# Kernel optimization log

Hardware: AMD Instinct MI355X
Metric: run time of the kernel (lower is better)

Reference implementation:

```python
import jax, jax.numpy as jnp
import numpy as np

N_NODES = 100000
N_EDGES = 1600000
NFEAT, NHID, NCLASS = 128, 64, 16


def setup_inputs() -> dict:
    key = jax.random.key(0)
    k1, k2, k3, k4, k5 = jax.random.split(key, 5)
    x = jax.random.normal(k1, (N_NODES, NFEAT), dtype=jnp.float32)
    edge_index = jax.random.randint(k2, (2, N_EDGES), 0, N_NODES, dtype=jnp.int64)
    edge_weight = jax.random.uniform(k3, (N_EDGES,), dtype=jnp.float32)
    # PyG Linear default init ~ kaiming-uniform; plain scaled normals suffice as a baseline
    W1 = jax.random.normal(k4, (NFEAT, NHID), dtype=jnp.float32) / np.sqrt(NFEAT)
    W2 = jax.random.normal(k5, (NHID, NCLASS), dtype=jnp.float32) / np.sqrt(NHID)
    return {"x": x, "edge_index": edge_index, "edge_weight": edge_weight, "W1": W1, "W2": W2}


def _gcn_conv(x, W, src, dst, w, num_nodes):
    # GCNConv(normalize=False, add_self_loops=False, bias=False):
    # out[dst] = sum_{e: dst(e)=dst} w_e * (x @ W)[src(e)]
    h = x @ W                                    # [N, out]
    msg = w[:, None] * h[src]                    # [E, out] gathered messages
    return jax.ops.segment_sum(msg, dst, num_segments=num_nodes)


def reference(x, edge_index, edge_weight, W1, W2):
    src, dst = edge_index[0], edge_index[1]
    h = jax.nn.relu(_gcn_conv(x, W1, src, dst, edge_weight, N_NODES))
    out = _gcn_conv(h, W2, src, dst, edge_weight, N_NODES)
    return out
```

## Files before the change

### kernel.cpp

```cpp
#include <hip/hip_runtime.h>

#define N_NODES 100000
#define N_EDGES 1600000
#define NFEAT 128
#define NHID 64
#define NCLASS 16

#define NPB 196
#define NB 511
#define HIST_EPT 16
#define HIST_BLOCKS ((N_EDGES + 256 * HIST_EPT - 1) / (256 * HIST_EPT))
#define FILL_EPT 8
#define FILL_BLOCKS ((N_EDGES + 256 * FILL_EPT - 1) / (256 * FILL_EPT))
#define NTILES ((N_NODES + 15) / 16)
#define GEMM_BLOCKS ((NTILES + 3) / 4)

typedef unsigned int u32;
typedef __attribute__((ext_vector_type(8))) short bf16x8;
typedef __attribute__((ext_vector_type(4))) float f32x4;

__device__ __forceinline__ u32 pack_bf16(float a, float b) {
    u32 ua = __float_as_uint(a);
    u32 ub = __float_as_uint(b);
    ua = (ua + 0x7fffu + ((ua >> 16) & 1u)) >> 16;
    ub = (ub + 0x7fffu + ((ub >> 16) & 1u)) >> 16;
    return ua | (ub << 16);
}
__device__ __forceinline__ short f2bf(float f) {
    u32 u = __float_as_uint(f);
    u = (u + 0x7fffu + ((u >> 16) & 1u)) >> 16;
    return (short)u;
}
__device__ __forceinline__ float bf16_lo(u32 u) { return __uint_as_float(u << 16); }
__device__ __forceinline__ float bf16_hi(u32 u) { return __uint_as_float(u & 0xffff0000u); }

__global__ void detect_kernel(const u32* __restrict__ ei, int* __restrict__ flag) {
    __shared__ int any_nz;
    if (threadIdx.x == 0) any_nz = 0;
    __syncthreads();
    u32 v = ei[2 * threadIdx.x + 1];
    if (v != 0) any_nz = 1;
    __syncthreads();
    if (threadIdx.x == 0) *flag = any_nz;
}

__device__ __forceinline__ int load_idx(const void* ei, int flag, size_t pos) {
    return flag ? ((const int*)ei)[pos] : (int)((const long long*)ei)[pos];
}

__global__ __launch_bounds__(256) void histA_kernel(const void* __restrict__ ei,
                                                    const int* __restrict__ flag,
                                                    int* __restrict__ ghist) {
    __shared__ int cnt[512];
    int t = threadIdx.x;
    cnt[t] = 0;
    cnt[t + 256] = 0;
    __syncthreads();
    int f = *flag;
    int base = blockIdx.x * 256 * HIST_EPT;
#pragma unroll
    for (int k = 0; k < HIST_EPT; ++k) {
        int e = base + k * 256 + t;
        if (e < N_EDGES) {
            int d = load_idx(ei, f, (size_t)N_EDGES + e);
            atomicAdd(&cnt[d / NPB], 1);
        }
    }
    __syncthreads();
    if (cnt[t] > 0) atomicAdd(&ghist[t], cnt[t]);
    if (cnt[t + 256] > 0) atomicAdd(&ghist[t + 256], cnt[t + 256]);
}

__global__ __launch_bounds__(512) void scanA_kernel(const int* __restrict__ ghist,
                                                    int* __restrict__ bstart,
                                                    int* __restrict__ gcursor) {
    __shared__ int lds[512];
    int t = threadIdx.x;
    int own = (t < NB) ? ghist[t] : 0;
    lds[t] = own;
    __syncthreads();
    for (int off = 1; off < 512; off <<= 1) {
        int v = (t >= off) ? lds[t - off] : 0;
        __syncthreads();
        lds[t] += v;
        __syncthreads();
    }
    int excl = lds[t] - own;
    bstart[t] = excl;
    if (t == 511) bstart[512] = lds[511];
    if (t < NB) gcursor[t] = excl;
}

__global__ __launch_bounds__(256) void fillA_kernel(const void* __restrict__ ei,
                                                    const int* __restrict__ flag,
                                                    const float* __restrict__ ew,
                                                    int* __restrict__ gcursor,
                                                    int2* __restrict__ ebuf) {
    __shared__ int cnt[512];
    __shared__ int base[512];
    int t = threadIdx.x;
    cnt[t] = 0;
    cnt[t + 256] = 0;
    __syncthreads();
    int f = *flag;
    int eb = blockIdx.x * 256 * FILL_EPT;
    int src[FILL_EPT], bin[FILL_EPT], rank[FILL_EPT];
    float w[FILL_EPT];
#pragma unroll
    for (int k = 0; k < FILL_EPT; ++k) {
        int e = eb + k * 256 + t;
        bin[k] = -1;
        if (e < N_EDGES) {
            int s = load_idx(ei, f, (size_t)e);
            int d = load_idx(ei, f, (size_t)N_EDGES + e);
            int b = d / NPB;
            src[k] = s | ((d - b * NPB) << 20);
            w[k] = ew[e];
            bin[k] = b;
            rank[k] = atomicAdd(&cnt[b], 1);
        }
    }
    __syncthreads();
    if (cnt[t] > 0) base[t] = atomicAdd(&gcursor[t], cnt[t]);
    if (cnt[t + 256] > 0) base[t + 256] = atomicAdd(&gcursor[t + 256], cnt[t + 256]);
    __syncthreads();
#pragma unroll
    for (int k = 0; k < FILL_EPT; ++k) {
        if (bin[k] >= 0) {
            int pos = base[bin[k]] + rank[k];
            ebuf[pos] = make_int2(src[k], __float_as_int(w[k]));
        }
    }
}

__global__ __launch_bounds__(256) void sortB_kernel(const int2* __restrict__ ebuf,
                                                    const int* __restrict__ bstart,
                                                    int2* __restrict__ ebuf2,
                                                    int* __restrict__ row_ptr) {
    __shared__ int cnt[NPB];
    __shared__ int sc[256];
    __shared__ int cur[NPB];
    int t = threadIdx.x, b = blockIdx.x;
    for (int i = t; i < NPB; i += 256) cnt[i] = 0;
    __syncthreads();
    int start = bstart[b], end = bstart[b + 1];
    for (int i = start + t; i < end; i += 256) {
        int dl = ((u32)ebuf[i].x) >> 20;
        atomicAdd(&cnt[dl], 1);
    }
    __syncthreads();
    int own = (t < NPB) ? cnt[t] : 0;
    sc[t] = own;
    __syncthreads();
    for (int off = 1; off < 256; off <<= 1) {
        int v = (t >= off) ? sc[t - off] : 0;
        __syncthreads();
        sc[t] += v;
        __syncthreads();
    }
    int excl = sc[t] - own;
    if (t < NPB) {
        cur[t] = excl;
        int node = b * NPB + t;
        if (node < N_NODES) row_ptr[node] = start + excl;
    }
    if (b == 0 && t == 0) row_ptr[N_NODES] = N_EDGES;
    __syncthreads();
    for (int i = start + t; i < end; i += 256) {
        int2 p = ebuf[i];
        int dl = ((u32)p.x) >> 20;
        int pos = start + atomicAdd(&cur[dl], 1);
        ebuf2[pos] = make_int2(p.x & 0xFFFFF, p.y);
    }
}

__global__ __launch_bounds__(256) void gemm1_kernel(const float* __restrict__ X,
                                                    const float* __restrict__ W,
                                                    u32* __restrict__ Y) {
    __shared__ float Wsh[NFEAT * NHID];
    int t = threadIdx.x;
    for (int i = t; i < NFEAT * NHID; i += 256) Wsh[i] = W[i];
    __syncthreads();
    int wid = t >> 6;
    int lane = t & 63;
    int r = lane & 15, g = lane >> 4;
    int m0 = (blockIdx.x * 4 + wid) * 16;
    if (m0 >= N_NODES) return;

    bf16x8 af[4][4];
#pragma unroll
    for (int nt = 0; nt < 4; ++nt)
#pragma unroll
        for (int kt = 0; kt < 4; ++kt)
#pragma unroll
            for (int j = 0; j < 8; ++j)
                af[nt][kt][j] = f2bf(Wsh[(kt * 32 + g * 8 + j) * NHID + nt * 16 + r]);

    const float* xr = X + (size_t)(m0 + r) * NFEAT + g * 8;
    bf16x8 bfr[4];
#pragma unroll
    for (int kt = 0; kt < 4; ++kt) {
        float4 v0 = *(const float4*)(xr + kt * 32);
        float4 v1 = *(const float4*)(xr + kt * 32 + 4);
        bfr[kt][0] = f2bf(v0.x); bfr[kt][1] = f2bf(v0.y);
        bfr[kt][2] = f2bf(v0.z); bfr[kt][3] = f2bf(v0.w);
        bfr[kt][4] = f2bf(v1.x); bfr[kt][5] = f2bf(v1.y);
        bfr[kt][6] = f2bf(v1.z); bfr[kt][7] = f2bf(v1.w);
    }

    u32* yr = Y + (size_t)(m0 + r) * (NHID / 2);
#pragma unroll
    for (int nt = 0; nt < 4; ++nt) {
        f32x4 acc = {0.f, 0.f, 0.f, 0.f};
#pragma unroll
        for (int kt = 0; kt < 4; ++kt)
            acc = __builtin_amdgcn_mfma_f32_16x16x32_bf16(af[nt][kt], bfr[kt], acc, 0, 0, 0);
        uint2 o;
        o.x = pack_bf16(acc[0], acc[1]);
        o.y = pack_bf16(acc[2], acc[3]);
        *(uint2*)(yr + nt * 8 + g * 2) = o;
    }
}

__global__ __launch_bounds__(256) void gemm2_kernel(const float* __restrict__ H,
                                                    const float* __restrict__ W,
                                                    u32* __restrict__ Y) {
    __shared__ float Wsh[NHID * NCLASS];
    int t = threadIdx.x;
    for (int i = t; i < NHID * NCLASS; i += 256) Wsh[i] = W[i];
    __syncthreads();
    int wid = t >> 6;
    int lane = t & 63;
    int r = lane & 15, g = lane >> 4;
    int m0 = (blockIdx.x * 4 + wid) * 16;
    if (m0 >= N_NODES) return;

    bf16x8 af[2];
#pragma unroll
    for (int kt = 0; kt < 2; ++kt)
#pragma unroll
        for (int j = 0; j < 8; ++j)
            af[kt][j] = f2bf(Wsh[(kt * 32 + g * 8 + j) * NCLASS + r]);

    const float* hr = H + (size_t)(m0 + r) * NHID + g * 8;
    bf16x8 bfr[2];
#pragma unroll
    for (int kt = 0; kt < 2; ++kt) {
        float4 v0 = *(const float4*)(hr + kt * 32);
        float4 v1 = *(const float4*)(hr + kt * 32 + 4);
        bfr[kt][0] = f2bf(v0.x); bfr[kt][1] = f2bf(v0.y);
        bfr[kt][2] = f2bf(v0.z); bfr[kt][3] = f2bf(v0.w);
        bfr[kt][4] = f2bf(v1.x); bfr[kt][5] = f2bf(v1.y);
        bfr[kt][6] = f2bf(v1.z); bfr[kt][7] = f2bf(v1.w);
    }

    f32x4 acc = {0.f, 0.f, 0.f, 0.f};
    acc = __builtin_amdgcn_mfma_f32_16x16x32_bf16(af[0], bfr[0], acc, 0, 0, 0);
    acc = __builtin_amdgcn_mfma_f32_16x16x32_bf16(af[1], bfr[1], acc, 0, 0, 0);

    u32* yr = Y + (size_t)(m0 + r) * (NCLASS / 2);
    uint2 o;
    o.x = pack_bf16(acc[0], acc[1]);
    o.y = pack_bf16(acc[2], acc[3]);
    *(uint2*)(yr + g * 2) = o;
}

__global__ __launch_bounds__(256) void agg1_kernel(const u32* __restrict__ xwb,
                                                   const int* __restrict__ row_ptr,
                                                   const int2* __restrict__ ep,
                                                   float* __restrict__ h) {
    int t = blockIdx.x * 256 + threadIdx.x;
    int node = t >> 5;
    int ln = t & 31;
    if (node >= N_NODES) return;
    int start = row_ptr[node], end = row_ptr[node + 1];
    float a0x = 0.f, a0y = 0.f, a1x = 0.f, a1y = 0.f;
    float a2x = 0.f, a2y = 0.f, a3x = 0.f, a3y = 0.f;
    int last = end - 1;
    for (int i = start; i < end; i += 4) {
        int i1 = min(i + 1, last), i2 = min(i + 2, last), i3 = min(i + 3, last);
        int2 p0 = ep[i];
        int2 p1 = ep[i1];
        int2 p2 = ep[i2];
        int2 p3 = ep[i3];
        u32 u0 = xwb[(size_t)p0.x * 32 + ln];
        u32 u1 = xwb[(size_t)p1.x * 32 + ln];
        u32 u2 = xwb[(size_t)p2.x * 32 + ln];
        u32 u3 = xwb[(size_t)p3.x * 32 + ln];
        float w0 = __int_as_float(p0.y);
        float w1 = (i + 1 < end) ? __int_as_float(p1.y) : 0.f;
        float w2 = (i + 2 < end) ? __int_as_float(p2.y) : 0.f;
        float w3 = (i + 3 < end) ? __int_as_float(p3.y) : 0.f;
        a0x += w0 * bf16_lo(u0); a0y += w0 * bf16_hi(u0);
        a1x += w1 * bf16_lo(u1); a1y += w1 * bf16_hi(u1);
        a2x += w2 * bf16_lo(u2); a2y += w2 * bf16_hi(u2);
        a3x += w3 * bf16_lo(u3); a3y += w3 * bf16_hi(u3);
    }
    float sx = (a0x + a1x) + (a2x + a3x);
    float sy = (a0y + a1y) + (a2y + a3y);
    *(float2*)(h + (size_t)node * NHID + 2 * ln) =
        make_float2(fmaxf(sx, 0.f), fmaxf(sy, 0.f));
}

__global__ __launch_bounds__(256) void agg2_kernel(const u32* __restrict__ hwb,
                                                   const int* __restrict__ row_ptr,
                                                   const int2* __restrict__ ep,
                                                   float* __restrict__ out) {
    int t = blockIdx.x * 256 + threadIdx.x;
    int node = t >> 6;
    int lane = t & 63;
    int p = lane & 7;
    int sub = lane >> 3;
    if (node >= N_NODES) return;
    int start = row_ptr[node], end = row_ptr[node + 1];
    float ax = 0.f, ay = 0.f;
    for (int i = start + sub; i < end; i += 8) {
        int2 pr = ep[i];
        u32 u = hwb[(size_t)pr.x * 8 + p];
        float w = __int_as_float(pr.y);
        ax += w * bf16_lo(u);
        ay += w * bf16_hi(u);
    }
    ax += __shfl_xor(ax, 8, 64);  ay += __shfl_xor(ay, 8, 64);
    ax += __shfl_xor(ax, 16, 64); ay += __shfl_xor(ay, 16, 64);
    ax += __shfl_xor(ax, 32, 64); ay += __shfl_xor(ay, 32, 64);
    if (sub == 0) *(float2*)(out + (size_t)node * NCLASS + 2 * p) = make_float2(ax, ay);
}

extern "C" void kernel_launch(void* const* d_in, const int* in_sizes, int n_in,
                              void* d_out, int out_size, void* d_ws, size_t ws_size,
                              hipStream_t stream) {
    const float* x  = (const float*)d_in[0];
    const void*  ei = d_in[1];
    const float* ew = (const float*)d_in[2];
    const float* W1 = (const float*)d_in[3];
    const float* W2 = (const float*)d_in[4];
    float* out = (float*)d_out;

    char* ws = (char*)d_ws;
    size_t off = 0;
    auto take = [&](size_t bytes) {
        char* p = ws + off;
        off += (bytes + 511) & ~(size_t)511;
        return p;
    };
    int*   flag    = (int*)take(4);
    int*   ghist   = (int*)take(512 * 4);
    int*   bstart  = (int*)take(513 * 4);
    int*   gcursor = (int*)take(512 * 4);
    int*   row_ptr = (int*)take((size_t)(N_NODES + 1) * 4);
    int2*  ebuf    = (int2*)take((size_t)N_EDGES * 8);
    int2*  ebuf2   = (int2*)take((size_t)N_EDGES * 8);
    u32*   xwb     = (u32*)take((size_t)N_NODES * (NHID / 2) * 4);
    float* h       = (float*)take((size_t)N_NODES * NHID * 4);
    u32*   hwb     = xwb;

    detect_kernel<<<1, 256, 0, stream>>>((const u32*)ei, flag);
    hipMemsetAsync(ghist, 0, 512 * 4, stream);
    histA_kernel<<<HIST_BLOCKS, 256, 0, stream>>>(ei, flag, ghist);
    scanA_kernel<<<1, 512, 0, stream>>>(ghist, bstart, gcursor);
    fillA_kernel<<<FILL_BLOCKS, 256, 0, stream>>>(ei, flag, ew, gcursor, ebuf);
    sortB_kernel<<<NB, 256, 0, stream>>>(ebuf, bstart, ebuf2, row_ptr);

    gemm1_kernel<<<GEMM_BLOCKS, 256, 0, stream>>>(x, W1, xwb);
    agg1_kernel<<<(N_NODES * 32 + 255) / 256, 256, 0, stream>>>(xwb, row_ptr, ebuf2, h);
    gemm2_kernel<<<GEMM_BLOCKS, 256, 0, stream>>>(h, W2, hwb);
    agg2_kernel<<<(N_NODES * 64 + 255) / 256, 256, 0, stream>>>(hwb, row_ptr, ebuf2, out);
}
```

Before: 172.7 us.

## Store hidden layer as bf16 and widen aggregation gathers with multi-edge lanes

agg1 now writes the ReLU hidden activations as packed bf16 instead of fp32, and gemm2 loads them directly as bf16x8 vectors, which halves that intermediate traffic and removes the conversion work. agg1 is remapped to 64 lanes per node: 16 feature lanes, each doing 8-byte gathers, and 4 edge sub-groups reduced with shuffles. agg2 likewise uses 8-byte gathers with 16 edge sub-groups per node and writes float4 outputs. The aim is to cut memory traffic and expose more edge-level parallelism. The cost is an extra bf16 rounding of h, plus more threads and shuffle reductions per node.

```diff
diff --git a/kernel.cpp b/kernel.cpp
--- a/kernel.cpp
+++ b/kernel.cpp
@@ -222,7 +222,7 @@
     }
 }
 
-__global__ __launch_bounds__(256) void gemm2_kernel(const float* __restrict__ H,
+__global__ __launch_bounds__(256) void gemm2_kernel(const u32* __restrict__ Hb,
                                                     const float* __restrict__ W,
                                                     u32* __restrict__ Y) {
     __shared__ float Wsh[NHID * NCLASS];
@@ -242,21 +242,13 @@
         for (int j = 0; j < 8; ++j)
             af[kt][j] = f2bf(Wsh[(kt * 32 + g * 8 + j) * NCLASS + r]);
 
-    const float* hr = H + (size_t)(m0 + r) * NHID + g * 8;
-    bf16x8 bfr[2];
-#pragma unroll
-    for (int kt = 0; kt < 2; ++kt) {
-        float4 v0 = *(const float4*)(hr + kt * 32);
-        float4 v1 = *(const float4*)(hr + kt * 32 + 4);
-        bfr[kt][0] = f2bf(v0.x); bfr[kt][1] = f2bf(v0.y);
-        bfr[kt][2] = f2bf(v0.z); bfr[kt][3] = f2bf(v0.w);
-        bfr[kt][4] = f2bf(v1.x); bfr[kt][5] = f2bf(v1.y);
-        bfr[kt][6] = f2bf(v1.z); bfr[kt][7] = f2bf(v1.w);
-    }
+    const u32* hr = Hb + (size_t)(m0 + r) * (NHID / 2) + g * 4;
+    bf16x8 b0 = *(const bf16x8*)(hr + 0);
+    bf16x8 b1 = *(const bf16x8*)(hr + 16);
 
     f32x4 acc = {0.f, 0.f, 0.f, 0.f};
-    acc = __builtin_amdgcn_mfma_f32_16x16x32_bf16(af[0], bfr[0], acc, 0, 0, 0);
-    acc = __builtin_amdgcn_mfma_f32_16x16x32_bf16(af[1], bfr[1], acc, 0, 0, 0);
+    acc = __builtin_amdgcn_mfma_f32_16x16x32_bf16(af[0], b0, acc, 0, 0, 0);
+    acc = __builtin_amdgcn_mfma_f32_16x16x32_bf16(af[1], b1, acc, 0, 0, 0);
 
     u32* yr = Y + (size_t)(m0 + r) * (NCLASS / 2);
     uint2 o;
@@ -268,38 +260,47 @@
 __global__ __launch_bounds__(256) void agg1_kernel(const u32* __restrict__ xwb,
                                                    const int* __restrict__ row_ptr,
                                                    const int2* __restrict__ ep,
-                                                   float* __restrict__ h) {
+                                                   u32* __restrict__ hb) {
     int t = blockIdx.x * 256 + threadIdx.x;
-    int node = t >> 5;
-    int ln = t & 31;
+    int node = t >> 6;
+    int lane = t & 63;
+    int p = lane & 15;
+    int sub = lane >> 4;
     if (node >= N_NODES) return;
     int start = row_ptr[node], end = row_ptr[node + 1];
-    float a0x = 0.f, a0y = 0.f, a1x = 0.f, a1y = 0.f;
-    float a2x = 0.f, a2y = 0.f, a3x = 0.f, a3y = 0.f;
-    int last = end - 1;
-    for (int i = start; i < end; i += 4) {
-        int i1 = min(i + 1, last), i2 = min(i + 2, last), i3 = min(i + 3, last);
-        int2 p0 = ep[i];
-        int2 p1 = ep[i1];
-        int2 p2 = ep[i2];
-        int2 p3 = ep[i3];
-        u32 u0 = xwb[(size_t)p0.x * 32 + ln];
-        u32 u1 = xwb[(size_t)p1.x * 32 + ln];
-        u32 u2 = xwb[(size_t)p2.x * 32 + ln];
-        u32 u3 = xwb[(size_t)p3.x * 32 + ln];
-        float w0 = __int_as_float(p0.y);
-        float w1 = (i + 1 < end) ? __int_as_float(p1.y) : 0.f;
-        float w2 = (i + 2 < end) ? __int_as_float(p2.y) : 0.f;
-        float w3 = (i + 3 < end) ? __int_as_float(p3.y) : 0.f;
-        a0x += w0 * bf16_lo(u0); a0y += w0 * bf16_hi(u0);
-        a1x += w1 * bf16_lo(u1); a1y += w1 * bf16_hi(u1);
-        a2x += w2 * bf16_lo(u2); a2y += w2 * bf16_hi(u2);
-        a3x += w3 * bf16_lo(u3); a3y += w3 * bf16_hi(u3);
-    }
-    float sx = (a0x + a1x) + (a2x + a3x);
-    float sy = (a0y + a1y) + (a2y + a3y);
-    *(float2*)(h + (size_t)node * NHID + 2 * ln) =
-        make_float2(fmaxf(sx, 0.f), fmaxf(sy, 0.f));
+    float f0 = 0.f, f1 = 0.f, f2 = 0.f, f3 = 0.f;
+    float g0 = 0.f, g1 = 0.f, g2 = 0.f, g3 = 0.f;
+    int i = start + sub;
+    for (; i + 4 < end; i += 8) {
+        int2 pa = ep[i];
+        int2 pb = ep[i + 4];
+        uint2 ua = *(const uint2*)(xwb + (size_t)pa.x * 32 + 2 * p);
+        uint2 ub = *(const uint2*)(xwb + (size_t)pb.x * 32 + 2 * p);
+        float wa = __int_as_float(pa.y);
+        float wb = __int_as_float(pb.y);
+        f0 += wa * bf16_lo(ua.x); f1 += wa * bf16_hi(ua.x);
+        f2 += wa * bf16_lo(ua.y); f3 += wa * bf16_hi(ua.y);
+        g0 += wb * bf16_lo(ub.x); g1 += wb * bf16_hi(ub.x);
+        g2 += wb * bf16_lo(ub.y); g3 += wb * bf16_hi(ub.y);
+    }
+    if (i < end) {
+        int2 pa = ep[i];
+        uint2 ua = *(const uint2*)(xwb + (size_t)pa.x * 32 + 2 * p);
+        float wa = __int_as_float(pa.y);
+        f0 += wa * bf16_lo(ua.x); f1 += wa * bf16_hi(ua.x);
+        f2 += wa * bf16_lo(ua.y); f3 += wa * bf16_hi(ua.y);
+    }
+    f0 += g0; f1 += g1; f2 += g2; f3 += g3;
+    f0 += __shfl_xor(f0, 16, 64); f1 += __shfl_xor(f1, 16, 64);
+    f2 += __shfl_xor(f2, 16, 64); f3 += __shfl_xor(f3, 16, 64);
+    f0 += __shfl_xor(f0, 32, 64); f1 += __shfl_xor(f1, 32, 64);
+    f2 += __shfl_xor(f2, 32, 64); f3 += __shfl_xor(f3, 32, 64);
+    if (sub == 0) {
+        uint2 o;
+        o.x = pack_bf16(fmaxf(f0, 0.f), fmaxf(f1, 0.f));
+        o.y = pack_bf16(fmaxf(f2, 0.f), fmaxf(f3, 0.f));
+        *(uint2*)(hb + (size_t)node * 32 + 2 * p) = o;
+    }
 }
 
 __global__ __launch_bounds__(256) void agg2_kernel(const u32* __restrict__ hwb,
@@ -309,22 +310,29 @@
     int t = blockIdx.x * 256 + threadIdx.x;
     int node = t >> 6;
     int lane = t & 63;
-    int p = lane & 7;
-    int sub = lane >> 3;
+    int p = lane & 3;
+    int sub = lane >> 2;
     if (node >= N_NODES) return;
     int start = row_ptr[node], end = row_ptr[node + 1];
-    float ax = 0.f, ay = 0.f;
-    for (int i = start + sub; i < end; i += 8) {
+    float f0 = 0.f, f1 = 0.f, f2 = 0.f, f3 = 0.f;
+    for (int i = start + sub; i < end; i += 16) {
         int2 pr = ep[i];
-        u32 u = hwb[(size_t)pr.x * 8 + p];
+        uint2 u = *(const uint2*)(hwb + (size_t)pr.x * 8 + 2 * p);
         float w = __int_as_float(pr.y);
-        ax += w * bf16_lo(u);
-        ay += w * bf16_hi(u);
-    }
-    ax += __shfl_xor(ax, 8, 64);  ay += __shfl_xor(ay, 8, 64);
-    ax += __shfl_xor(ax, 16, 64); ay += __shfl_xor(ay, 16, 64);
-    ax += __shfl_xor(ax, 32, 64); ay += __shfl_xor(ay, 32, 64);
-    if (sub == 0) *(float2*)(out + (size_t)node * NCLASS + 2 * p) = make_float2(ax, ay);
+        f0 += w * bf16_lo(u.x); f1 += w * bf16_hi(u.x);
+        f2 += w * bf16_lo(u.y); f3 += w * bf16_hi(u.y);
+    }
+    f0 += __shfl_xor(f0, 4, 64);  f1 += __shfl_xor(f1, 4, 64);
+    f2 += __shfl_xor(f2, 4, 64);  f3 += __shfl_xor(f3, 4, 64);
+    f0 += __shfl_xor(f0, 8, 64);  f1 += __shfl_xor(f1, 8, 64);
+    f2 += __shfl_xor(f2, 8, 64);  f3 += __shfl_xor(f3, 8, 64);
+    f0 += __shfl_xor(f0, 16, 64); f1 += __shfl_xor(f1, 16, 64);
+    f2 += __shfl_xor(f2, 16, 64); f3 += __shfl_xor(f3, 16, 64);
+    f0 += __shfl_xor(f0, 32, 64); f1 += __shfl_xor(f1, 32, 64);
+    f2 += __shfl_xor(f2, 32, 64); f3 += __shfl_xor(f3, 32, 64);
+    if (sub == 0) {
+        *(float4*)(out + (size_t)node * NCLASS + 4 * p) = make_float4(f0, f1, f2, f3);
+    }
 }
 
 extern "C" void kernel_launch(void* const* d_in, const int* in_sizes, int n_in,
@@ -352,7 +360,7 @@
     int2*  ebuf    = (int2*)take((size_t)N_EDGES * 8);
     int2*  ebuf2   = (int2*)take((size_t)N_EDGES * 8);
     u32*   xwb     = (u32*)take((size_t)N_NODES * (NHID / 2) * 4);
-    float* h       = (float*)take((size_t)N_NODES * NHID * 4);
+    u32*   hb      = (u32*)take((size_t)N_NODES * (NHID / 2) * 4);
     u32*   hwb     = xwb;
 
     detect_kernel<<<1, 256, 0, stream>>>((const u32*)ei, flag);
@@ -363,7 +371,7 @@
     sortB_kernel<<<NB, 256, 0, stream>>>(ebuf, bstart, ebuf2, row_ptr);
 
     gemm1_kernel<<<GEMM_BLOCKS, 256, 0, stream>>>(x, W1, xwb);
-    agg1_kernel<<<(N_NODES * 32 + 255) / 256, 256, 0, stream>>>(xwb, row_ptr, ebuf2, h);
-    gemm2_kernel<<<GEMM_BLOCKS, 256, 0, stream>>>(h, W2, hwb);
+    agg1_kernel<<<(N_NODES * 64 + 255) / 256, 256, 0, stream>>>(xwb, row_ptr, ebuf2, hb);
+    gemm2_kernel<<<GEMM_BLOCKS, 256, 0, stream>>>(hb, W2, hwb);
     agg2_kernel<<<(N_NODES * 64 + 255) / 256, 256, 0, stream>>>(hwb, row_ptr, ebuf2, out);
 }
```

Measured after the change: 168.7 us. -2.3%, faster.
